# Performance work log

Hardware: AMD Instinct MI355X
Metric: run time of the kernel (lower is better)

## Reference

```python
import jax, jax.numpy as jnp
import numpy as np

N = 1_000_000      # number of observed reflections
DMETA = 32         # metadata feature dim


def setup_inputs() -> dict:
    key = jax.random.key(0)
    k1, k2, k3, k4 = jax.random.split(key, 4)
    # positive Miller indices so gcd >= 1 (avoids division by zero)
    hkl = jax.random.randint(k1, (N, 3), 1, 51, dtype=jnp.int32)
    # resolutions in [1, 3) Angstrom, dmin = 1.0 -> 1..3 harmonics typically
    dHKL = 1.0 + 2.0 * jax.random.uniform(k2, (N, 1), dtype=jnp.float32)
    # Laue wavelength band [0.8, 1.2) Angstrom
    wavelength = 0.8 + 0.4 * jax.random.uniform(k3, (N, 1), dtype=jnp.float32)
    meta = jax.random.normal(k4, (N, DMETA), dtype=jnp.float32)
    dmin = jnp.float32(1.0)  # registered buffer in the torch module
    return {"hkl": hkl, "dHKL": dHKL, "wavelength": wavelength,
            "meta": meta, "dmin": dmin}


def _expand_indices(hkl, dHKL, dmin):
    """gcd reduction, harmonic count, and the (row idx, harmonic order) compaction."""
    g = jnp.gcd(jnp.gcd(hkl[:, 0], hkl[:, 1]), hkl[:, 2])[:, None]  # [N,1]
    d0 = dHKL * g.astype(dHKL.dtype)                                 # [N,1]
    n_max = jnp.floor_divide(d0, dmin).astype(jnp.int32)[:, 0]       # [N]
    n_big = int(n_max.max())                                         # device sync (as in torch)
    harm = jnp.arange(1, n_big + 2)                                  # [H] values 1..n_max.max()+1
    mask = harm[None, :] <= n_max[:, None]                           # [N,H]
    idx, col = jnp.nonzero(mask)                                     # ragged compaction (eager)
    n_obs = col + 1                                                  # harmonic order, 1-based
    return g, d0, idx, n_obs


def reference(hkl, dHKL, wavelength, meta, dmin):
    g, d0, idx, n_obs = _expand_indices(hkl, dHKL, dmin)
    hkl_0 = hkl // g                                   # fundamental Miller indices
    wavelength_0 = wavelength * g.astype(wavelength.dtype)
    nf = n_obs[:, None].astype(d0.dtype)
    hkl_out = hkl_0[idx] * n_obs[:, None]              # [M,3]
    dHKL_out = d0[idx] / nf                            # [M,1]
    wavelength_out = wavelength_0[idx] / nf            # [M,1]
    meta_out = meta[idx]                               # [M,DMETA]
    return hkl_out, dHKL_out, wavelength_out, meta_out
```

## Files before the change

kernel.cpp:

```cpp
#include <hip/hip_runtime.h>


typedef float f32x4 __attribute__((ext_vector_type(4)));

__device__ __forceinline__ int gcd2(int a, int b) {
    while (b) { int t = a % b; a = b; b = t; }
    return a;
}
__device__ __forceinline__ int gcd3(int a, int b, int c) {
    return gcd2(gcd2(a, b), c);
}

__device__ __forceinline__ int row_nmax(const int* __restrict__ hkl,
                                        const float* __restrict__ dHKL,
                                        float dmin, int i, int* g_out) {
    int h = hkl[3 * i], k = hkl[3 * i + 1], l = hkl[3 * i + 2];
    int g = gcd3(h, k, l);
    *g_out = g;
    float d0 = dHKL[i] * (float)g;
    return (int)floorf(d0 / dmin);
}

__global__ void k_count(const int* __restrict__ hkl, const float* __restrict__ dHKL,
                        const float* __restrict__ dmin_p,
                        int* __restrict__ bsums, int N) {
    int i = blockIdx.x * 256 + threadIdx.x;
    int nm = 0;
    if (i < N) {
        int g;
        nm = row_nmax(hkl, dHKL, dmin_p[0], i, &g);
    }
    __shared__ int red[256];
    red[threadIdx.x] = nm;
    __syncthreads();
    for (int s = 128; s > 0; s >>= 1) {
        if (threadIdx.x < s) red[threadIdx.x] += red[threadIdx.x + s];
        __syncthreads();
    }
    if (threadIdx.x == 0) bsums[blockIdx.x] = red[0];
}

__global__ void k_scan(const int* __restrict__ bsums, int* __restrict__ boffs, int nb) {
    __shared__ int tmp[1024];
    __shared__ int carry;
    if (threadIdx.x == 0) carry = 0;
    __syncthreads();
    for (int t0 = 0; t0 < nb; t0 += 1024) {
        int idx = t0 + threadIdx.x;
        int v = (idx < nb) ? bsums[idx] : 0;
        tmp[threadIdx.x] = v;
        __syncthreads();
        for (int off = 1; off < 1024; off <<= 1) {
            int x = (threadIdx.x >= off) ? tmp[threadIdx.x - off] : 0;
            __syncthreads();
            tmp[threadIdx.x] += x;
            __syncthreads();
        }
        int inc = tmp[threadIdx.x];
        if (idx < nb) boffs[idx] = carry + inc - v;
        __syncthreads();
        if (threadIdx.x == 1023) carry += inc;
        __syncthreads();
    }
}

__global__ void k_expand(const int* __restrict__ hkl, const float* __restrict__ dHKL,
                         const float* __restrict__ dmin_p, const int* __restrict__ boffs,
                         int* __restrict__ pack, int N, int M) {
    int tid = threadIdx.x;
    int i = blockIdx.x * 256 + tid;
    int nm = 0, g;
    if (i < N) nm = row_nmax(hkl, dHKL, dmin_p[0], i, &g);
    __shared__ int tmp[256];
    tmp[tid] = nm;
    __syncthreads();
    for (int off = 1; off < 256; off <<= 1) {
        int x = (tid >= off) ? tmp[tid - off] : 0;
        __syncthreads();
        tmp[tid] += x;
        __syncthreads();
    }
    int base = boffs[blockIdx.x] + tmp[tid] - nm;
    if (i < N) {
        int p = (i << 8);
        for (int n = 1; n <= nm; n++) {
            int m = base + n - 1;
            if (m < M) pack[m] = p | n;
        }
    }
}

__global__ void k_scalar(const int* __restrict__ pack, const int* __restrict__ hkl,
                         const float* __restrict__ dHKL, const float* __restrict__ wl,
                         float* __restrict__ out, int M, int N) {
    int m = blockIdx.x * 256 + threadIdx.x;
    if (m >= M) return;
    int p = pack[m];
    int row = p >> 8;
    int n = p & 255;
    if (row >= N || row < 0 || n == 0) { row = 0; n = 1; }
    int h = hkl[3 * row], k = hkl[3 * row + 1], l = hkl[3 * row + 2];
    int g = gcd3(h, k, l);
    float gf = (float)g;
    float nf = (float)n;
    __builtin_nontemporal_store((float)((h / g) * n), &out[3 * m]);
    __builtin_nontemporal_store((float)((k / g) * n), &out[3 * m + 1]);
    __builtin_nontemporal_store((float)((l / g) * n), &out[3 * m + 2]);
    __builtin_nontemporal_store((dHKL[row] * gf) / nf, &out[(size_t)3 * M + m]);
    __builtin_nontemporal_store((wl[row] * gf) / nf,   &out[(size_t)4 * M + m]);
}

__global__ void k_meta4(const int* __restrict__ pack, const float* __restrict__ meta,
                        float* __restrict__ out5, int total, int pad,
                        int nbody4, int nextra, int N) {
    int t = blockIdx.x * 256 + threadIdx.x;
    if (t < nbody4) {
        int p = pad + (t << 2);
        int m0 = p >> 5;
        int ra = pack[m0] >> 8;
        if (ra >= N || ra < 0) ra = 0;
        f32x4 v;
        if (pad == 0) {
            const f32x4* meta4 = (const f32x4*)meta;
            v = meta4[(ra << 3) + ((p & 31) >> 2)];
        } else {
            int m3 = (p + 3) >> 5;
            int rb = (m3 == m0) ? ra : (pack[m3] >> 8);
            if (rb >= N || rb < 0) rb = 0;
            {
                int pj = p;     int mj = pj >> 5; int rj = (mj == m0) ? ra : rb;
                v.x = meta[(rj << 5) + (pj & 31)];
            }
            {
                int pj = p + 1; int mj = pj >> 5; int rj = (mj == m0) ? ra : rb;
                v.y = meta[(rj << 5) + (pj & 31)];
            }
            {
                int pj = p + 2; int mj = pj >> 5; int rj = (mj == m0) ? ra : rb;
                v.z = meta[(rj << 5) + (pj & 31)];
            }
            {
                int pj = p + 3; int mj = pj >> 5; int rj = (mj == m0) ? ra : rb;
                v.w = meta[(rj << 5) + (pj & 31)];
            }
        }
        __builtin_nontemporal_store(v, (f32x4*)(out5 + p));
    } else {
        int e = t - nbody4;
        if (e < nextra) {
            int p = (e < pad) ? e : (pad + (nbody4 << 2) + (e - pad));
            if (p < total) {
                int m = p >> 5;
                int r = pack[m] >> 8;
                if (r >= N || r < 0) r = 0;
                __builtin_nontemporal_store(meta[(r << 5) + (p & 31)], out5 + p);
            }
        }
    }
}

extern "C" void kernel_launch(void* const* d_in, const int* in_sizes, int n_in,
                              void* d_out, int out_size, void* d_ws, size_t ws_size,
                              hipStream_t stream) {
    const int*   hkl  = (const int*)d_in[0];
    const float* dHKL = (const float*)d_in[1];
    const float* wl   = (const float*)d_in[2];
    const float* meta = (const float*)d_in[3];
    const float* dmin = (const float*)d_in[4];
    float* out = (float*)d_out;

    int N = in_sizes[0] / 3;
    int M = out_size / 37;
    int nb = (N + 255) / 256;

    int* bsums = (int*)d_ws;
    int* boffs = bsums + nb;
    int* pack  = boffs + nb;

    k_count<<<nb, 256, 0, stream>>>(hkl, dHKL, dmin, bsums, N);
    k_scan<<<1, 1024, 0, stream>>>(bsums, boffs, nb);
    k_expand<<<nb, 256, 0, stream>>>(hkl, dHKL, dmin, boffs, pack, N, M);

    int g4 = (M + 255) / 256;
    k_scalar<<<g4, 256, 0, stream>>>(pack, hkl, dHKL, wl, out, M, N);

    int total = 32 * M;
    int base  = 5 * M;
    int pad   = (4 - (base & 3)) & 3;
    if (pad > total) pad = total;
    int body   = total - pad;
    int nbody4 = body >> 2;
    int tail   = body & 3;
    int nextra = pad + tail;
    int g5 = (nbody4 + nextra + 255) / 256;
    k_meta4<<<g5, 256, 0, stream>>>(pack, meta, out + (size_t)5 * M,
                                    total, pad, nbody4, nextra, N);
}
```

Baseline: 526.7 us.

## Cache gcd/nmax per row, fuse scalar outputs into expand, use wave-shuffle scans

k_count now stores the gcd and harmonic count per row in a workspace array, so k_expand no longer recomputes the gcd. k_expand writes the hkl, dHKL and wavelength outputs directly while expanding, which removes the separate k_scalar kernel and its gather through pack. The block reductions and scans switch from shared-memory loops with many barriers to wavefront shuffles. The trade-off is that the per-row loop in k_expand issues strided, uncoalesced stores and its work is uneven across threads, and it uses extra workspace of N ints.

```diff
diff --git a/kernel.cpp b/kernel.cpp
--- a/kernel.cpp
+++ b/kernel.cpp
@@ -11,103 +11,100 @@
     return gcd2(gcd2(a, b), c);
 }
 
-__device__ __forceinline__ int row_nmax(const int* __restrict__ hkl,
-                                        const float* __restrict__ dHKL,
-                                        float dmin, int i, int* g_out) {
-    int h = hkl[3 * i], k = hkl[3 * i + 1], l = hkl[3 * i + 2];
-    int g = gcd3(h, k, l);
-    *g_out = g;
-    float d0 = dHKL[i] * (float)g;
-    return (int)floorf(d0 / dmin);
-}
-
 __global__ void k_count(const int* __restrict__ hkl, const float* __restrict__ dHKL,
                         const float* __restrict__ dmin_p,
-                        int* __restrict__ bsums, int N) {
-    int i = blockIdx.x * 256 + threadIdx.x;
+                        int* __restrict__ rowinfo, int* __restrict__ bsums, int N) {
+    int tid = threadIdx.x;
+    int i = blockIdx.x * 256 + tid;
+    int lane = tid & 63, wave = tid >> 6;
     int nm = 0;
     if (i < N) {
-        int g;
-        nm = row_nmax(hkl, dHKL, dmin_p[0], i, &g);
+        int h = hkl[3 * i], k = hkl[3 * i + 1], l = hkl[3 * i + 2];
+        int g = gcd3(h, k, l);
+        float d0 = dHKL[i] * (float)g;
+        nm = (int)floorf(d0 / dmin_p[0]);
+        rowinfo[i] = (nm << 8) | g;
     }
-    __shared__ int red[256];
-    red[threadIdx.x] = nm;
+    int v = nm;
+    #pragma unroll
+    for (int off = 32; off > 0; off >>= 1) v += __shfl_down(v, off);
+    __shared__ int ws4[4];
+    if (lane == 0) ws4[wave] = v;
     __syncthreads();
-    for (int s = 128; s > 0; s >>= 1) {
-        if (threadIdx.x < s) red[threadIdx.x] += red[threadIdx.x + s];
-        __syncthreads();
-    }
-    if (threadIdx.x == 0) bsums[blockIdx.x] = red[0];
+    if (tid == 0) bsums[blockIdx.x] = ws4[0] + ws4[1] + ws4[2] + ws4[3];
 }
 
 __global__ void k_scan(const int* __restrict__ bsums, int* __restrict__ boffs, int nb) {
-    __shared__ int tmp[1024];
-    __shared__ int carry;
-    if (threadIdx.x == 0) carry = 0;
+    __shared__ int wsums[16];
+    __shared__ int carry_s;
+    int tid = threadIdx.x, lane = tid & 63, wave = tid >> 6;
+    if (tid == 0) carry_s = 0;
     __syncthreads();
     for (int t0 = 0; t0 < nb; t0 += 1024) {
-        int idx = t0 + threadIdx.x;
-        int v = (idx < nb) ? bsums[idx] : 0;
-        tmp[threadIdx.x] = v;
+        int idx = t0 + tid;
+        int orig = (idx < nb) ? bsums[idx] : 0;
+        int v = orig;
+        #pragma unroll
+        for (int off = 1; off < 64; off <<= 1) {
+            int x = __shfl_up(v, off);
+            if (lane >= off) v += x;
+        }
+        if (lane == 63) wsums[wave] = v;
         __syncthreads();
-        for (int off = 1; off < 1024; off <<= 1) {
-            int x = (threadIdx.x >= off) ? tmp[threadIdx.x - off] : 0;
-            __syncthreads();
-            tmp[threadIdx.x] += x;
-            __syncthreads();
-        }
-        int inc = tmp[threadIdx.x];
-        if (idx < nb) boffs[idx] = carry + inc - v;
+        int wbase = 0;
+        #pragma unroll
+        for (int w = 0; w < 16; w++) wbase += (w < wave) ? wsums[w] : 0;
+        int carry = carry_s;
         __syncthreads();
-        if (threadIdx.x == 1023) carry += inc;
+        if (idx < nb) boffs[idx] = carry + wbase + v - orig;
+        if (tid == 1023) carry_s = carry + wbase + v;
         __syncthreads();
     }
 }
 
 __global__ void k_expand(const int* __restrict__ hkl, const float* __restrict__ dHKL,
-                         const float* __restrict__ dmin_p, const int* __restrict__ boffs,
-                         int* __restrict__ pack, int N, int M) {
+                         const float* __restrict__ wl, const int* __restrict__ rowinfo,
+                         const int* __restrict__ boffs, int* __restrict__ pack,
+                         float* __restrict__ out, int N, int M) {
     int tid = threadIdx.x;
     int i = blockIdx.x * 256 + tid;
-    int nm = 0, g;
-    if (i < N) nm = row_nmax(hkl, dHKL, dmin_p[0], i, &g);
-    __shared__ int tmp[256];
-    tmp[tid] = nm;
+    int lane = tid & 63, wave = tid >> 6;
+    int info = (i < N) ? rowinfo[i] : 0;
+    int nm = info >> 8;
+    int g  = info & 255;
+    int v = nm;
+    #pragma unroll
+    for (int off = 1; off < 64; off <<= 1) {
+        int x = __shfl_up(v, off);
+        if (lane >= off) v += x;
+    }
+    __shared__ int ws4[4];
+    if (lane == 63) ws4[wave] = v;
     __syncthreads();
-    for (int off = 1; off < 256; off <<= 1) {
-        int x = (tid >= off) ? tmp[tid - off] : 0;
-        __syncthreads();
-        tmp[tid] += x;
-        __syncthreads();
-    }
-    int base = boffs[blockIdx.x] + tmp[tid] - nm;
-    if (i < N) {
+    int wbase = 0;
+    #pragma unroll
+    for (int w = 0; w < 4; w++) wbase += (w < wave) ? ws4[w] : 0;
+    int base = boffs[blockIdx.x] + wbase + v - nm;
+
+    if (i < N && nm > 0) {
+        int h = hkl[3 * i], k = hkl[3 * i + 1], l = hkl[3 * i + 2];
+        int h0 = h / g, k0 = k / g, l0 = l / g;
+        float dg = dHKL[i] * (float)g;
+        float wg = wl[i] * (float)g;
         int p = (i << 8);
         for (int n = 1; n <= nm; n++) {
             int m = base + n - 1;
-            if (m < M) pack[m] = p | n;
+            if (m < M) {
+                float nf = (float)n;
+                pack[m] = p | n;
+                __builtin_nontemporal_store((float)(h0 * n), &out[3 * m]);
+                __builtin_nontemporal_store((float)(k0 * n), &out[3 * m + 1]);
+                __builtin_nontemporal_store((float)(l0 * n), &out[3 * m + 2]);
+                __builtin_nontemporal_store(dg / nf, &out[(size_t)3 * M + m]);
+                __builtin_nontemporal_store(wg / nf, &out[(size_t)4 * M + m]);
+            }
         }
     }
-}
-
-__global__ void k_scalar(const int* __restrict__ pack, const int* __restrict__ hkl,
-                         const float* __restrict__ dHKL, const float* __restrict__ wl,
-                         float* __restrict__ out, int M, int N) {
-    int m = blockIdx.x * 256 + threadIdx.x;
-    if (m >= M) return;
-    int p = pack[m];
-    int row = p >> 8;
-    int n = p & 255;
-    if (row >= N || row < 0 || n == 0) { row = 0; n = 1; }
-    int h = hkl[3 * row], k = hkl[3 * row + 1], l = hkl[3 * row + 2];
-    int g = gcd3(h, k, l);
-    float gf = (float)g;
-    float nf = (float)n;
-    __builtin_nontemporal_store((float)((h / g) * n), &out[3 * m]);
-    __builtin_nontemporal_store((float)((k / g) * n), &out[3 * m + 1]);
-    __builtin_nontemporal_store((float)((l / g) * n), &out[3 * m + 2]);
-    __builtin_nontemporal_store((dHKL[row] * gf) / nf, &out[(size_t)3 * M + m]);
-    __builtin_nontemporal_store((wl[row] * gf) / nf,   &out[(size_t)4 * M + m]);
 }
 
 __global__ void k_meta4(const int* __restrict__ pack, const float* __restrict__ meta,
@@ -173,16 +170,14 @@
     int M = out_size / 37;
     int nb = (N + 255) / 256;
 
-    int* bsums = (int*)d_ws;
-    int* boffs = bsums + nb;
-    int* pack  = boffs + nb;
+    int* rowinfo = (int*)d_ws;
+    int* bsums   = rowinfo + N;
+    int* boffs   = bsums + nb;
+    int* pack    = boffs + nb;
 
-    k_count<<<nb, 256, 0, stream>>>(hkl, dHKL, dmin, bsums, N);
+    k_count<<<nb, 256, 0, stream>>>(hkl, dHKL, dmin, rowinfo, bsums, N);
     k_scan<<<1, 1024, 0, stream>>>(bsums, boffs, nb);
-    k_expand<<<nb, 256, 0, stream>>>(hkl, dHKL, dmin, boffs, pack, N, M);
-
-    int g4 = (M + 255) / 256;
-    k_scalar<<<g4, 256, 0, stream>>>(pack, hkl, dHKL, wl, out, M, N);
+    k_expand<<<nb, 256, 0, stream>>>(hkl, dHKL, wl, rowinfo, boffs, pack, out, N, M);
 
     int total = 32 * M;
     int base  = 5 * M;
```

Measured after the change: 597.6 us. 1.13x slower.
